# Performance work log

Hardware: AMD Instinct MI355X
Metric: run time of the kernel (lower is better)

The kernel has to match this reference:

```python
import jax, jax.numpy as jnp
import numpy as np
from jax import lax

ALPHA = float(np.exp(-1.0 / 5.0))   # exp(-1/tau_mem), tau_mem=5.0
THRESHOLD = 1.0


def _dwconv(x, w, b, groups):
    # x: (B, Cin, T), w: (Cout, Cin/groups, K), 'same' padding for odd K
    pad = (w.shape[-1] - 1) // 2
    y = lax.conv_general_dilated(
        x, w, window_strides=(1,), padding=[(pad, pad)],
        dimension_numbers=("NCH", "OIH", "NCH"), feature_group_count=groups)
    return y + b[None, :, None]


def setup_inputs() -> dict:
    key = jax.random.key(0)
    ks = jax.random.split(key, 12)
    B, C, T = 8, 256, 4096
    OP = 6            # out_per_kernel for each of the 3 kernel sizes
    DEC = 128         # decoder_channels
    f32 = jnp.float32
    d = {}
    d["x"] = jax.random.normal(ks[0], (B, C, T), f32)
    # depthwise multi-path conv params (groups=C): weight (C*OP, 1, K)
    d["w3"] = jax.random.normal(ks[1], (C * OP, 1, 3), f32) * 0.2
    d["b3"] = jnp.zeros((C * OP,), f32)
    d["w5"] = jax.random.normal(ks[2], (C * OP, 1, 5), f32) * 0.15
    d["b5"] = jnp.zeros((C * OP,), f32)
    d["w9"] = jax.random.normal(ks[3], (C * OP, 1, 9), f32) * 0.1
    d["b9"] = jnp.zeros((C * OP,), f32)
    # reduce: Conv1d(C*18 -> C, k=1, groups=C): weight (C, 18, 1)
    d["w_red"] = jax.random.normal(ks[4], (C, 3 * OP, 1), f32) * 0.2
    d["b_red"] = jnp.zeros((C,), f32)
    d["latency_scale"] = jnp.asarray(5.0, f32)
    # output_gates: xavier uniform (C, C) with zero diagonal
    bound = float(np.sqrt(6.0 / (C + C)))
    og = jax.random.uniform(ks[5], (C, C), f32, -bound, bound)
    d["output_gates"] = og * (1.0 - jnp.eye(C, dtype=f32))
    d["bias"] = jnp.zeros((C,), f32)
    # post_mlp: Linear(C, DEC) -> ReLU -> Linear(DEC, C); stored as (in, out)
    d["W1"] = jax.random.normal(ks[6], (C, DEC), f32) * float(np.sqrt(2.0 / C))
    d["b1"] = jnp.zeros((DEC,), f32)
    d["W2"] = jax.random.normal(ks[7], (DEC, C), f32) * float(np.sqrt(2.0 / DEC))
    d["b2"] = jnp.zeros((C,), f32)
    return d


def reference(x, w3, b3, w5, b5, w9, b9, w_red, b_red,
              latency_scale, output_gates, bias, W1, b1, W2, b2):
    B, C, T = x.shape
    # DepthwiseMultiPathEncoder: 3 depthwise convs -> cat -> grouped 1x1 reduce
    o3 = _dwconv(x, w3, b3, C)
    o5 = _dwconv(x, w5, b5, C)
    o9 = _dwconv(x, w9, b9, C)
    cat = jnp.concatenate([o3, o5, o9], axis=1)      # (B, 18C, T)
    drive = _dwconv(cat, w_red, b_red, C)             # (B, C, T)
    # LIF membrane recurrence + first-spike latency (sequential over T)
    d_t = jnp.moveaxis(drive, 2, 0)                   # (T, B, C)
    def step(V, dt):
        V = ALPHA * V + (1.0 - ALPHA) * dt
        return V, V >= THRESHOLD
    _, crossed = lax.scan(step, jnp.zeros((B, C), x.dtype), d_t)  # (T, B, C) bool
    fired_any = crossed.any(axis=0)
    first_t = jnp.argmax(crossed, axis=0)             # first True index
    true_latency = jnp.where(fired_any, first_t, T).astype(x.dtype)  # (B, C)
    # latency -> activation -> gated mix -> MLP -> softplus, clamp [0, T]
    scale = jnp.maximum(latency_scale, 0.001)
    act = jnp.exp(-true_latency / scale)              # (B, C)
    mixed = act @ output_gates.T + bias[None, :]      # (B, C)
    h = jax.nn.relu(mixed @ W1 + b1)
    raw_pred = h @ W2 + b2
    pred_latency = jnp.clip(jax.nn.softplus(raw_pred), 0.0, float(T))
    return pred_latency, true_latency, act
```

## Files before the change

kernel.cpp:

```cpp
#include <hip/hip_runtime.h>
#include <math.h>

#define C_CH 256
#define T_LEN 4096


__global__ __launch_bounds__(512, 8) void drive_scan_kernel(
    const float* __restrict__ x,
    const float* __restrict__ w3, const float* __restrict__ b3,
    const float* __restrict__ w5, const float* __restrict__ b5,
    const float* __restrict__ w9, const float* __restrict__ b9,
    const float* __restrict__ w_red, const float* __restrict__ b_red,
    const float* __restrict__ latency_scale,
    const float* __restrict__ og, const float* __restrict__ W1,
    const float* __restrict__ W2, float* __restrict__ sink,
    float* __restrict__ out_lat, float* __restrict__ out_act)
{
    const int blk = blockIdx.x;
    const int tid = threadIdx.x;

    if (blk >= 2048) {
        const int id = (blk - 2048) * 512 + tid;
        float acc = 0.0f;
        const float4* og4 = (const float4*)og;
        const float4* W14 = (const float4*)W1;
        const float4* W24 = (const float4*)W2;
        #pragma unroll
        for (int v = 0; v < 4; ++v) {
            float4 q = og4[id + v * 4096]; acc += q.x + q.y + q.z + q.w;
        }
        #pragma unroll
        for (int v = 0; v < 2; ++v) {
            float4 q = W14[id + v * 4096]; acc += q.x + q.y + q.z + q.w;
        }
        #pragma unroll
        for (int v = 0; v < 2; ++v) {
            float4 q = W24[id + v * 4096]; acc += q.x + q.y + q.z + q.w;
        }
        sink[id] = acc;
        return;
    }

    const int b    = blk >> 8;
    const int c    = blk & 255;
    const int lane = tid & 63;
    const int wv   = tid >> 6;

    __shared__ float sWF[28];
    __shared__ float sHalo[2][8][512];
    __shared__ float sWaveTot[8];
    __shared__ float sCarry[8];
    __shared__ int   sMin[8];

    if (tid < 27) {
        const int r = tid / 9, k = tid - 9 * r;
        const int q0     = 18 * c + 6 * r;
        const int region = (q0 >= 1536) + (q0 >= 3072);
        const int p0     = q0 - region * 1536;
        const int K      = (region == 0) ? 3 : (region == 1 ? 5 : 9);
        const int off    = (9 - K) >> 1;
        const float* wP  = (region == 0) ? w3 : (region == 1 ? w5 : w9);
        const int kk     = k - off;
        float w = 0.0f;
        if (kk >= 0 && kk < K) {
            const float* wr = w_red + c * 18 + 6 * r;
            #pragma unroll
            for (int j = 0; j < 6; ++j)
                w = fmaf(wr[j], wP[(p0 + j) * K + kk], w);
        }
        sWF[tid] = w;
    } else if (tid == 27) {
        float acc = b_red[c];
        #pragma unroll
        for (int r = 0; r < 3; ++r) {
            const int q0     = 18 * c + 6 * r;
            const int region = (q0 >= 1536) + (q0 >= 3072);
            const int p0     = q0 - region * 1536;
            const float* bP  = (region == 0) ? b3 : (region == 1 ? b5 : b9);
            const float* wr  = w_red + c * 18 + 6 * r;
            #pragma unroll
            for (int j = 0; j < 6; ++j) acc = fmaf(wr[j], bP[p0 + j], acc);
        }
        sWF[27] = acc;
    }

    const int t0 = tid << 3;
    float d[8];
    float Beff;
    #pragma unroll
    for (int r = 0; r < 3; ++r) {
        const int buf = r & 1;
        const int src = (3 * c + r) & 255;
        const float4* p = (const float4*)(x + ((size_t)b * C_CH + src) * T_LEN + t0);
        float xa[16];
        {
            float4 q0 = p[0], q1 = p[1];
            xa[4] = q0.x; xa[5] = q0.y; xa[6]  = q0.z; xa[7]  = q0.w;
            xa[8] = q1.x; xa[9] = q1.y; xa[10] = q1.z; xa[11] = q1.w;
        }
        #pragma unroll
        for (int e = 0; e < 8; ++e) sHalo[buf][e][tid] = xa[4 + e];
        __syncthreads();
        if (r == 0) {
            Beff = sWF[27];
            #pragma unroll
            for (int tt = 0; tt < 8; ++tt) d[tt] = Beff;
        }
        #pragma unroll
        for (int e = 0; e < 4; ++e)
            xa[e] = tid ? sHalo[buf][4 + e][tid - 1] : 0.0f;
        #pragma unroll
        for (int e = 0; e < 4; ++e)
            xa[12 + e] = (tid < 511) ? sHalo[buf][e][tid + 1] : 0.0f;
        #pragma unroll
        for (int k = 0; k < 9; ++k) {
            const float wk = sWF[r * 9 + k];
            #pragma unroll
            for (int tt = 0; tt < 8; ++tt)
                d[tt] = fmaf(wk, xa[tt + k], d[tt]);
        }
    }

    const float A   = (float)0.8187307530779818;
    const float OMA = (float)(1.0 - 0.8187307530779818);

    float S = 0.0f;
    #pragma unroll
    for (int tt = 0; tt < 8; ++tt) S = A * S + OMA * d[tt];

    const float Fp[6] = {
        (float)2.0189651799465541e-01,
        (float)4.0762203978366215e-02,
        (float)1.6615572731739337e-03,
        (float)2.7607725720371943e-06,
        (float)7.6218649302532563e-12,
        (float)5.8092835977683129e-23
    };
    float cinc = S;
    #pragma unroll
    for (int s = 0; s < 6; ++s) {
        const int o = 1 << s;
        const float y = __shfl_up(cinc, o, 64);
        if (lane >= o) cinc = fmaf(Fp[s], y, cinc);
    }
    if (lane == 63) sWaveTot[wv] = cinc;
    __syncthreads();
    if (tid == 0) {
        const float A512 = 3.3744728758705166e-45f;
        float g = 0.0f;
        #pragma unroll
        for (int w = 0; w < 8; ++w) { sCarry[w] = g; g = sWaveTot[w] + A512 * g; }
    }
    __syncthreads();
    const float cprev = __shfl_up(cinc, 1, 64);
    const float Vin = (lane ? cprev : 0.0f)
                    + expf(-1.6f * (float)lane) * sCarry[wv];

    float V = Vin;
    int firstT = T_LEN;
    #pragma unroll
    for (int tt = 0; tt < 8; ++tt) {
        V = A * V + OMA * d[tt];
        if (V >= 1.0f && firstT == T_LEN) firstT = t0 + tt;
    }

    #pragma unroll
    for (int o = 32; o > 0; o >>= 1)
        firstT = min(firstT, __shfl_xor(firstT, o, 64));
    if (lane == 0) sMin[wv] = firstT;
    __syncthreads();
    if (tid == 0) {
        int f = sMin[0];
        #pragma unroll
        for (int w = 1; w < 8; ++w) f = min(f, sMin[w]);
        const float lat   = (float)f;
        const float scale = fmaxf(latency_scale[0], 0.001f);
        out_lat[blk] = lat;
        out_act[blk] = expf(-lat / scale);
    }
}

__global__ __launch_bounds__(512) void mlp_kernel(
    const float* __restrict__ act,
    const float* __restrict__ og, const float* __restrict__ bias,
    const float* __restrict__ W1, const float* __restrict__ b1,
    const float* __restrict__ W2, const float* __restrict__ b2,
    float* __restrict__ out_pred)
{
    const int b = blockIdx.x;
    const int t = threadIdx.x;
    const int j = t & 255;
    const int g = t >> 8;

    __shared__ float sAct[256];
    __shared__ float sOg[2][32][257];
    __shared__ float sP[2][256];
    __shared__ float sMix[256];
    __shared__ float sPH[4][128];
    __shared__ float sH[128];
    __shared__ float sPR[2][256];

    if (t < 256) sAct[t] = act[b * 256 + t];

    float mix = 0.0f;
    for (int m = 0; m < 4; ++m) {
        const int i0 = g * 128 + m * 32;
        __syncthreads();
        #pragma unroll
        for (int q = 0; q < 32; ++q) {
            const int f  = (q << 8) + j;
            const int jj = f >> 5;
            const int ii = f & 31;
            sOg[g][ii][jj] = og[jj * 256 + i0 + ii];
        }
        __syncthreads();
        #pragma unroll
        for (int ii = 0; ii < 32; ++ii)
            mix = fmaf(sAct[i0 + ii], sOg[g][ii][j], mix);
    }
    sP[g][j] = mix;
    __syncthreads();
    if (t < 256) sMix[t] = bias[t] + sP[0][t] + sP[1][t];
    __syncthreads();

    {
        const int j1  = t & 127;
        const int seg = t >> 7;
        float h = 0.0f;
        #pragma unroll
        for (int ii = 0; ii < 64; ++ii) {
            const int i = seg * 64 + ii;
            h = fmaf(sMix[i], W1[i * 128 + j1], h);
        }
        sPH[seg][j1] = h;
    }
    __syncthreads();
    if (t < 128)
        sH[t] = fmaxf(b1[t] + ((sPH[0][t] + sPH[1][t]) + (sPH[2][t] + sPH[3][t])), 0.0f);
    __syncthreads();

    {
        float raw = 0.0f;
        #pragma unroll
        for (int kk = 0; kk < 64; ++kk) {
            const int k = g * 64 + kk;
            raw = fmaf(sH[k], W2[k * 256 + j], raw);
        }
        sPR[g][j] = raw;
    }
    __syncthreads();
    if (t < 256) {
        const float r  = b2[t] + sPR[0][t] + sPR[1][t];
        const float sp = fmaxf(r, 0.0f) + log1pf(expf(-fabsf(r)));
        out_pred[b * 256 + t] = fminf(fmaxf(sp, 0.0f), 4096.0f);
    }
}

extern "C" void kernel_launch(void* const* d_in, const int* in_sizes, int n_in,
                              void* d_out, int out_size, void* d_ws, size_t ws_size,
                              hipStream_t stream) {
    const float* x    = (const float*)d_in[0];
    const float* w3   = (const float*)d_in[1];
    const float* b3   = (const float*)d_in[2];
    const float* w5   = (const float*)d_in[3];
    const float* b5   = (const float*)d_in[4];
    const float* w9   = (const float*)d_in[5];
    const float* b9   = (const float*)d_in[6];
    const float* wred = (const float*)d_in[7];
    const float* bred = (const float*)d_in[8];
    const float* ls   = (const float*)d_in[9];
    const float* og   = (const float*)d_in[10];
    const float* bias = (const float*)d_in[11];
    const float* W1   = (const float*)d_in[12];
    const float* b1   = (const float*)d_in[13];
    const float* W2   = (const float*)d_in[14];
    const float* b2   = (const float*)d_in[15];

    float* sink     = (float*)d_ws;
    float* out      = (float*)d_out;
    float* out_pred = out;
    float* out_lat  = out + 2048;
    float* out_act  = out + 4096;

    drive_scan_kernel<<<2056, 512, 0, stream>>>(
        x, w3, b3, w5, b5, w9, b9, wred, bred, ls,
        og, W1, W2, sink, out_lat, out_act);
    mlp_kernel<<<8, 512, 0, stream>>>(out_act, og, bias, W1, b1, W2, b2, out_pred);
}
```

Baseline: 125.6 us.

## Fuse MLP into scan kernel via global atomic counter spin-wait

Merges the separate MLP kernel into the scan kernel. The last 8 blocks prefetch the weights, then spin on a global atomic counter until all 2048 scan blocks have published their latency and activation, and then run the gated-mix MLP in place. Shared memory is reorganised as a union so both roles fit. This removes a second kernel launch and its launch gap, but adds a hipMemsetAsync and relies on the 8 tail blocks not starving scan blocks of residency. Spin-waiting could deadlock if scheduling order differs.

```diff
diff --git a/kernel.cpp b/kernel.cpp
--- a/kernel.cpp
+++ b/kernel.cpp
@@ -5,39 +5,139 @@
 #define T_LEN 4096
 
 
-__global__ __launch_bounds__(512, 8) void drive_scan_kernel(
+union SharedU {
+    struct {
+        float halo[2][8][512];
+        float wf[28];
+        float wavetot[8];
+        float carry[8];
+        int   smin[8];
+    } d;
+    struct {
+        float act[256];
+        union {
+            float og[32][257];
+            struct { float ph[4][128]; float pr[2][256]; } w;
+        } u;
+        float p[2][256];
+        float mixv[256];
+        float hh[128];
+    } m;
+};
+
+__global__ __launch_bounds__(512, 8) void fused_kernel(
     const float* __restrict__ x,
     const float* __restrict__ w3, const float* __restrict__ b3,
     const float* __restrict__ w5, const float* __restrict__ b5,
     const float* __restrict__ w9, const float* __restrict__ b9,
     const float* __restrict__ w_red, const float* __restrict__ b_red,
     const float* __restrict__ latency_scale,
-    const float* __restrict__ og, const float* __restrict__ W1,
-    const float* __restrict__ W2, float* __restrict__ sink,
-    float* __restrict__ out_lat, float* __restrict__ out_act)
+    const float* __restrict__ og, const float* __restrict__ bias,
+    const float* __restrict__ W1, const float* __restrict__ b1,
+    const float* __restrict__ W2, const float* __restrict__ b2,
+    float* __restrict__ sink, int* __restrict__ counter,
+    float* __restrict__ out_pred, float* __restrict__ out_lat,
+    float* __restrict__ out_act)
 {
     const int blk = blockIdx.x;
     const int tid = threadIdx.x;
+    __shared__ SharedU su;
 
     if (blk >= 2048) {
-        const int id = (blk - 2048) * 512 + tid;
-        float acc = 0.0f;
-        const float4* og4 = (const float4*)og;
-        const float4* W14 = (const float4*)W1;
-        const float4* W24 = (const float4*)W2;
-        #pragma unroll
-        for (int v = 0; v < 4; ++v) {
-            float4 q = og4[id + v * 4096]; acc += q.x + q.y + q.z + q.w;
-        }
-        #pragma unroll
-        for (int v = 0; v < 2; ++v) {
-            float4 q = W14[id + v * 4096]; acc += q.x + q.y + q.z + q.w;
-        }
-        #pragma unroll
-        for (int v = 0; v < 2; ++v) {
-            float4 q = W24[id + v * 4096]; acc += q.x + q.y + q.z + q.w;
-        }
-        sink[id] = acc;
+        const int b = blk - 2048;
+        const int t = tid;
+        const int j = t & 255;
+        const int g = t >> 8;
+
+        {
+            float acc = 0.0f;
+            const int id = b * 512 + t;
+            const float4* og4 = (const float4*)og;
+            const float4* W14 = (const float4*)W1;
+            const float4* W24 = (const float4*)W2;
+            #pragma unroll
+            for (int v = 0; v < 4; ++v) {
+                float4 q = og4[id + v * 4096]; acc += q.x + q.y + q.z + q.w;
+            }
+            #pragma unroll
+            for (int v = 0; v < 2; ++v) {
+                float4 q = W14[id + v * 4096]; acc += q.x + q.y + q.z + q.w;
+            }
+            #pragma unroll
+            for (int v = 0; v < 2; ++v) {
+                float4 q = W24[id + v * 4096]; acc += q.x + q.y + q.z + q.w;
+            }
+            sink[id] = acc;
+        }
+
+        if (t == 0) {
+            while (__hip_atomic_load(counter, __ATOMIC_RELAXED,
+                                     __HIP_MEMORY_SCOPE_AGENT) != 2048)
+                __builtin_amdgcn_s_sleep(2);
+        }
+        __syncthreads();
+        __atomic_signal_fence(__ATOMIC_SEQ_CST);
+
+        if (t < 256)
+            su.m.act[t] = __hip_atomic_load(&out_act[b * 256 + t],
+                                            __ATOMIC_RELAXED,
+                                            __HIP_MEMORY_SCOPE_AGENT);
+
+        float mix = 0.0f;
+        for (int m8 = 0; m8 < 8; ++m8) {
+            const int i0 = m8 * 32;
+            __syncthreads();
+            #pragma unroll
+            for (int q = 0; q < 16; ++q) {
+                const int f  = (q << 9) + t;
+                const int jj = f >> 5;
+                const int ii = f & 31;
+                su.m.u.og[ii][jj] = og[jj * 256 + i0 + ii];
+            }
+            __syncthreads();
+            if ((m8 >> 2) == g) {
+                #pragma unroll
+                for (int ii = 0; ii < 32; ++ii)
+                    mix = fmaf(su.m.act[i0 + ii], su.m.u.og[ii][j], mix);
+            }
+        }
+        su.m.p[g][j] = mix;
+        __syncthreads();
+        if (t < 256) su.m.mixv[t] = bias[t] + su.m.p[0][t] + su.m.p[1][t];
+        __syncthreads();
+
+        {
+            const int j1  = t & 127;
+            const int seg = t >> 7;
+            float h = 0.0f;
+            #pragma unroll
+            for (int ii = 0; ii < 64; ++ii) {
+                const int i = seg * 64 + ii;
+                h = fmaf(su.m.mixv[i], W1[i * 128 + j1], h);
+            }
+            su.m.u.w.ph[seg][j1] = h;
+        }
+        __syncthreads();
+        if (t < 128)
+            su.m.hh[t] = fmaxf(b1[t] + ((su.m.u.w.ph[0][t] + su.m.u.w.ph[1][t])
+                                      + (su.m.u.w.ph[2][t] + su.m.u.w.ph[3][t])), 0.0f);
+        __syncthreads();
+
+        {
+            float raw = 0.0f;
+            #pragma unroll
+            for (int kk = 0; kk < 64; ++kk) {
+                const int k = g * 64 + kk;
+                raw = fmaf(su.m.hh[k], W2[k * 256 + j], raw);
+            }
+            su.m.u.w.pr[g][j] = raw;
+        }
+        __syncthreads();
+        if (t < 256) {
+            const float r  = b2[t] + su.m.u.w.pr[0][t] + su.m.u.w.pr[1][t];
+            const float sp = fmaxf(r, 0.0f) + log1pf(expf(-fabsf(r)));
+            out_pred[b * 256 + t] = fminf(fmaxf(sp, 0.0f), 4096.0f);
+        }
         return;
     }
 
@@ -45,12 +145,6 @@
     const int c    = blk & 255;
     const int lane = tid & 63;
     const int wv   = tid >> 6;
-
-    __shared__ float sWF[28];
-    __shared__ float sHalo[2][8][512];
-    __shared__ float sWaveTot[8];
-    __shared__ float sCarry[8];
-    __shared__ int   sMin[8];
 
     if (tid < 27) {
         const int r = tid / 9, k = tid - 9 * r;
@@ -68,7 +162,7 @@
             for (int j = 0; j < 6; ++j)
                 w = fmaf(wr[j], wP[(p0 + j) * K + kk], w);
         }
-        sWF[tid] = w;
+        su.d.wf[tid] = w;
     } else if (tid == 27) {
         float acc = b_red[c];
         #pragma unroll
@@ -81,7 +175,7 @@
             #pragma unroll
             for (int j = 0; j < 6; ++j) acc = fmaf(wr[j], bP[p0 + j], acc);
         }
-        sWF[27] = acc;
+        su.d.wf[27] = acc;
     }
 
     const int t0 = tid << 3;
@@ -99,22 +193,22 @@
             xa[8] = q1.x; xa[9] = q1.y; xa[10] = q1.z; xa[11] = q1.w;
         }
         #pragma unroll
-        for (int e = 0; e < 8; ++e) sHalo[buf][e][tid] = xa[4 + e];
+        for (int e = 0; e < 8; ++e) su.d.halo[buf][e][tid] = xa[4 + e];
         __syncthreads();
         if (r == 0) {
-            Beff = sWF[27];
+            Beff = su.d.wf[27];
             #pragma unroll
             for (int tt = 0; tt < 8; ++tt) d[tt] = Beff;
         }
         #pragma unroll
         for (int e = 0; e < 4; ++e)
-            xa[e] = tid ? sHalo[buf][4 + e][tid - 1] : 0.0f;
+            xa[e] = tid ? su.d.halo[buf][4 + e][tid - 1] : 0.0f;
         #pragma unroll
         for (int e = 0; e < 4; ++e)
-            xa[12 + e] = (tid < 511) ? sHalo[buf][e][tid + 1] : 0.0f;
+            xa[12 + e] = (tid < 511) ? su.d.halo[buf][e][tid + 1] : 0.0f;
         #pragma unroll
         for (int k = 0; k < 9; ++k) {
-            const float wk = sWF[r * 9 + k];
+            const float wk = su.d.wf[r * 9 + k];
             #pragma unroll
             for (int tt = 0; tt < 8; ++tt)
                 d[tt] = fmaf(wk, xa[tt + k], d[tt]);
@@ -143,18 +237,18 @@
         const float y = __shfl_up(cinc, o, 64);
         if (lane >= o) cinc = fmaf(Fp[s], y, cinc);
     }
-    if (lane == 63) sWaveTot[wv] = cinc;
+    if (lane == 63) su.d.wavetot[wv] = cinc;
     __syncthreads();
     if (tid == 0) {
         const float A512 = 3.3744728758705166e-45f;
         float g = 0.0f;
         #pragma unroll
-        for (int w = 0; w < 8; ++w) { sCarry[w] = g; g = sWaveTot[w] + A512 * g; }
+        for (int w = 0; w < 8; ++w) { su.d.carry[w] = g; g = su.d.wavetot[w] + A512 * g; }
     }
     __syncthreads();
     const float cprev = __shfl_up(cinc, 1, 64);
     const float Vin = (lane ? cprev : 0.0f)
-                    + expf(-1.6f * (float)lane) * sCarry[wv];
+                    + expf(-1.6f * (float)lane) * su.d.carry[wv];
 
     float V = Vin;
     int firstT = T_LEN;
@@ -167,92 +261,23 @@
     #pragma unroll
     for (int o = 32; o > 0; o >>= 1)
         firstT = min(firstT, __shfl_xor(firstT, o, 64));
-    if (lane == 0) sMin[wv] = firstT;
+    if (lane == 0) su.d.smin[wv] = firstT;
     __syncthreads();
     if (tid == 0) {
-        int f = sMin[0];
-        #pragma unroll
-        for (int w = 1; w < 8; ++w) f = min(f, sMin[w]);
+        int f = su.d.smin[0];
+        #pragma unroll
+        for (int w = 1; w < 8; ++w) f = min(f, su.d.smin[w]);
         const float lat   = (float)f;
         const float scale = fmaxf(latency_scale[0], 0.001f);
-        out_lat[blk] = lat;
-        out_act[blk] = expf(-lat / scale);
-    }
-}
-
-__global__ __launch_bounds__(512) void mlp_kernel(
-    const float* __restrict__ act,
-    const float* __restrict__ og, const float* __restrict__ bias,
-    const float* __restrict__ W1, const float* __restrict__ b1,
-    const float* __restrict__ W2, const float* __restrict__ b2,
-    float* __restrict__ out_pred)
-{
-    const int b = blockIdx.x;
-    const int t = threadIdx.x;
-    const int j = t & 255;
-    const int g = t >> 8;
-
-    __shared__ float sAct[256];
-    __shared__ float sOg[2][32][257];
-    __shared__ float sP[2][256];
-    __shared__ float sMix[256];
-    __shared__ float sPH[4][128];
-    __shared__ float sH[128];
-    __shared__ float sPR[2][256];
-
-    if (t < 256) sAct[t] = act[b * 256 + t];
-
-    float mix = 0.0f;
-    for (int m = 0; m < 4; ++m) {
-        const int i0 = g * 128 + m * 32;
-        __syncthreads();
-        #pragma unroll
-        for (int q = 0; q < 32; ++q) {
-            const int f  = (q << 8) + j;
-            const int jj = f >> 5;
-            const int ii = f & 31;
-            sOg[g][ii][jj] = og[jj * 256 + i0 + ii];
-        }
-        __syncthreads();
-        #pragma unroll
-        for (int ii = 0; ii < 32; ++ii)
-            mix = fmaf(sAct[i0 + ii], sOg[g][ii][j], mix);
-    }
-    sP[g][j] = mix;
-    __syncthreads();
-    if (t < 256) sMix[t] = bias[t] + sP[0][t] + sP[1][t];
-    __syncthreads();
-
-    {
-        const int j1  = t & 127;
-        const int seg = t >> 7;
-        float h = 0.0f;
-        #pragma unroll
-        for (int ii = 0; ii < 64; ++ii) {
-            const int i = seg * 64 + ii;
-            h = fmaf(sMix[i], W1[i * 128 + j1], h);
-        }
-        sPH[seg][j1] = h;
-    }
-    __syncthreads();
-    if (t < 128)
-        sH[t] = fmaxf(b1[t] + ((sPH[0][t] + sPH[1][t]) + (sPH[2][t] + sPH[3][t])), 0.0f);
-    __syncthreads();
-
-    {
-        float raw = 0.0f;
-        #pragma unroll
-        for (int kk = 0; kk < 64; ++kk) {
-            const int k = g * 64 + kk;
-            raw = fmaf(sH[k], W2[k * 256 + j], raw);
-        }
-        sPR[g][j] = raw;
-    }
-    __syncthreads();
-    if (t < 256) {
-        const float r  = b2[t] + sPR[0][t] + sPR[1][t];
-        const float sp = fmaxf(r, 0.0f) + log1pf(expf(-fabsf(r)));
-        out_pred[b * 256 + t] = fminf(fmaxf(sp, 0.0f), 4096.0f);
+        __hip_atomic_store(&out_lat[blk], lat, __ATOMIC_RELAXED,
+                           __HIP_MEMORY_SCOPE_AGENT);
+        __hip_atomic_store(&out_act[blk], expf(-lat / scale), __ATOMIC_RELAXED,
+                           __HIP_MEMORY_SCOPE_AGENT);
+        __atomic_signal_fence(__ATOMIC_SEQ_CST);
+        __builtin_amdgcn_s_waitcnt(0x0f70);
+        __atomic_signal_fence(__ATOMIC_SEQ_CST);
+        __hip_atomic_fetch_add(counter, 1, __ATOMIC_RELAXED,
+                               __HIP_MEMORY_SCOPE_AGENT);
     }
 }
 
@@ -276,14 +301,16 @@
     const float* W2   = (const float*)d_in[14];
     const float* b2   = (const float*)d_in[15];
 
-    float* sink     = (float*)d_ws;
+    int*   counter  = (int*)d_ws;
+    float* sink     = (float*)d_ws + 1024;
     float* out      = (float*)d_out;
     float* out_pred = out;
     float* out_lat  = out + 2048;
     float* out_act  = out + 4096;
 
-    drive_scan_kernel<<<2056, 512, 0, stream>>>(
+    hipMemsetAsync(counter, 0, 4, stream);
+    fused_kernel<<<2056, 512, 0, stream>>>(
         x, w3, b3, w5, b5, w9, b9, wred, bred, ls,
-        og, W1, W2, sink, out_lat, out_act);
-    mlp_kernel<<<8, 512, 0, stream>>>(out_act, og, bias, W1, b1, W2, b2, out_pred);
+        og, bias, W1, b1, W2, b2, sink, counter,
+        out_pred, out_lat, out_act);
 }
```

Measured after the change: 179.0 us. 1.43x slower.
